# Kernel tuning notes

Measured on AMD Instinct MI355X. Metric: run time of the kernel, lower is better.

## Reference

```python
import jax, jax.numpy as jnp
import numpy as np

B, N, D, H = 16, 256, 128, 8
HD = D // H
PAIR_DIMS = [64, 64, 64]
EPS = 1e-8


def _pairwise_lv_fts(x):
    # x: [B, 4, N] four-vectors (px, py, pz, E); returns [B, N, N, 4] = (lnkt, lnz, lndelta, lnm2)
    px, py, pz, e = x[:, 0], x[:, 1], x[:, 2], x[:, 3]
    pt = jnp.sqrt(jnp.clip(px ** 2 + py ** 2, EPS))          # [B, N]
    rap = 0.5 * jnp.log1p(2.0 * pz / jnp.clip(e - pz, 1e-20))
    phi = jnp.arctan2(py, px)
    d_rap = rap[:, :, None] - rap[:, None, :]                 # [B, N, N]
    d_phi = (phi[:, :, None] - phi[:, None, :] + np.pi) % (2.0 * np.pi) - np.pi
    delta = jnp.sqrt(d_rap ** 2 + d_phi ** 2)
    lndelta = jnp.log(jnp.clip(delta, EPS))
    ptmin = jnp.minimum(pt[:, :, None], pt[:, None, :])
    lnkt = jnp.log(jnp.clip(ptmin * delta, EPS))
    lnz = jnp.log(jnp.clip(ptmin / jnp.clip(pt[:, :, None] + pt[:, None, :], EPS), EPS))
    es = e[:, :, None] + e[:, None, :]
    pxs = px[:, :, None] + px[:, None, :]
    pys = py[:, :, None] + py[:, None, :]
    pzs = pz[:, :, None] + pz[:, None, :]
    lnm2 = jnp.log(jnp.clip(es ** 2 - pxs ** 2 - pys ** 2 - pzs ** 2, EPS))
    return jnp.stack([lnkt, lnz, lndelta, lnm2], axis=-1)


def setup_inputs() -> dict:
    key = jax.random.key(0)
    ks = jax.random.split(key, 12)
    p3 = jax.random.normal(ks[0], (B, 3, N), jnp.float32)
    e = jnp.sqrt((p3 ** 2).sum(1, keepdims=True)
                 + jnp.abs(jax.random.normal(ks[1], (B, 1, N), jnp.float32)) ** 2 + 0.1)
    x_pf = jnp.concatenate([p3, e], axis=1)                   # physical four-vectors [B,4,N]
    x_feat = jax.random.normal(ks[2], (B, N, D), jnp.float32) * 0.02
    dims = [4] + PAIR_DIMS + [H]
    pw = {}
    for i in range(4):
        pw[f"pair_w{i}"] = jax.random.normal(ks[3 + i], (dims[i], dims[i + 1]), jnp.float32) / np.sqrt(dims[i])
        pw[f"pair_b{i}"] = jnp.zeros((dims[i + 1],), jnp.float32)
    proj = {n: jax.random.normal(k, (D, D), jnp.float32) / np.sqrt(D)
            for n, k in zip(["wq", "wk", "wv", "wo"], jax.random.split(ks[7], 4))}
    bias = {n: jnp.zeros((D,), jnp.float32) for n in ["bq", "bk", "bv", "bo"]}
    return dict(x_pf=x_pf, x_feat=x_feat, **pw, **proj, **bias)


def reference(x_pf, x_feat, pair_w0, pair_b0, pair_w1, pair_b1, pair_w2, pair_b2,
              pair_w3, pair_b3, wq, wk, wv, wo, bq, bk, bv, bo):
    # pairwise Lorentz-invariant features -> dense attention bias
    u = _pairwise_lv_fts(x_pf)                                # [B, N, N, 4]
    for w, b in ((pair_w0, pair_b0), (pair_w1, pair_b1), (pair_w2, pair_b2)):
        u = jax.nn.gelu(u @ w + b)
    attn_bias = jnp.transpose(u @ pair_w3 + pair_b3, (0, 3, 1, 2))  # [B, H, N, N]
    # multi-head attention with pairwise bias
    q = (x_feat @ wq + bq).reshape(B, N, H, HD)
    k = (x_feat @ wk + bk).reshape(B, N, H, HD)
    v = (x_feat @ wv + bv).reshape(B, N, H, HD)
    scores = jnp.einsum("bihd,bjhd->bhij", q, k) / np.sqrt(HD) + attn_bias
    attn = jax.nn.softmax(scores, axis=-1)
    out = jnp.einsum("bhij,bjhd->bihd", attn, v).reshape(B, N, D)
    return out @ wo + bo                                      # [B, N, D]
```

## Files before the change

kernel.cpp:

```cpp
#include <hip/hip_runtime.h>
#include <hip/hip_bf16.h>
#include <math.h>

#define B_ 16
#define N_ 256
#define D_ 128
#define H_ 8
#define HD_ 16
#define EPS_ 1e-8f
#define PI_F 3.14159265358979323846f
#define TWO_PI_F 6.28318530717958647692f
#define INV_TWO_PI_F 0.15915494309189533577f
#define L2E_F 1.4426950408889634f

#define OFF_PT   0
#define OFF_RAP  4096
#define OFF_PHI  8192
#define OFF_PX   12288
#define OFF_PY   16384
#define OFF_PZ   20480
#define OFF_E    24576
#define OFF_Q    28672
#define OFF_BIAS (28672 + 3*524288)
#define OFF_AO   (OFF_BIAS + 8388608)
#define OFF_WPACK (OFF_AO + 524288)

#define UA0  0
#define UA1H 2048
#define UA1L 6144
#define UA2H 10240
#define UA2L 14336
#define UA3H 18432
#define UA3L 19456
#define UQKV 20480

typedef _Float16 f16x8 __attribute__((ext_vector_type(8)));
typedef _Float16 f16x4 __attribute__((ext_vector_type(4)));
typedef _Float16 f16x2 __attribute__((ext_vector_type(2)));
typedef __attribute__((ext_vector_type(4))) float f4;
typedef __attribute__((ext_vector_type(4))) unsigned int u4;

__device__ __forceinline__ unsigned pkh2(float a, float b) {
    f16x2 v = { (_Float16)a, (_Float16)b };
    return __builtin_bit_cast(unsigned, v);
}
__device__ __forceinline__ float f16res(float x) {
    return x - (float)(_Float16)x;
}

__device__ __forceinline__ float gelu_f(float x) {
    float y2 = x * fmaf(0.10294337f, x * x, 2.3022079f);
    float e = __builtin_amdgcn_exp2f(-y2);
    return x * __builtin_amdgcn_rcpf(1.0f + e);
}


__global__ __launch_bounds__(256) void k_prep(
    const float* __restrict__ w0, const float* __restrict__ w1,
    const float* __restrict__ w2, const float* __restrict__ w3,
    const float* __restrict__ wq, const float* __restrict__ wk,
    const float* __restrict__ wv, const float* __restrict__ wo,
    const float* __restrict__ x_pf,
    _Float16* __restrict__ wp, float* __restrict__ ws) {
    if (blockIdx.x >= 64) {
        int idx = (blockIdx.x - 64) * 256 + threadIdx.x;
        int b = idx >> 8, n = idx & 255;
        const float* base = x_pf + (size_t)b * 4 * N_;
        float px = base[0 * N_ + n];
        float py = base[1 * N_ + n];
        float pz = base[2 * N_ + n];
        float e  = base[3 * N_ + n];
        float pt  = sqrtf(fmaxf(px * px + py * py, EPS_));
        float rap = 0.5f * log1pf(2.0f * pz / fmaxf(e - pz, 1e-20f));
        float phi = atan2f(py, px);
        ws[OFF_PT  + idx] = pt;
        ws[OFF_RAP + idx] = rap;
        ws[OFF_PHI + idx] = phi;
        ws[OFF_PX  + idx] = px;
        ws[OFF_PY  + idx] = py;
        ws[OFF_PZ  + idx] = pz;
        ws[OFF_E   + idx] = e;
        return;
    }
    int id0 = blockIdx.x * 256 + threadIdx.x;
    const int gs = 64 * 256;
    for (int e = id0; e < 2048; e += gs) {
        int fi = e >> 3, j = e & 7;
        int mt = fi >> 6, lane = fi & 63;
        int q = lane >> 4, ln = lane & 15;
        int m = mt * 16 + ln;
        _Float16 v = (_Float16)0.0f;
        if (q == 0) v = (j < 4) ? (_Float16)w0[j * 64 + m]
                                : (_Float16)f16res(w0[(j - 4) * 64 + m]);
        else if (q == 1) v = (j < 4) ? (_Float16)w0[j * 64 + m] : (_Float16)0.0f;
        wp[UA0 + e] = v;
    }
    for (int e = id0; e < 4096; e += gs) {
        int fi = e >> 3, j = e & 7;
        int mt = fi >> 7, ks = (fi >> 6) & 1, lane = fi & 63;
        int q = lane >> 4;
        int m = mt * 16 + (lane & 15);
        int k = (2 * (j >> 2) + ks) * 16 + q * 4 + (j & 3);
        float x1 = w1[k * 64 + m];
        wp[UA1H + e] = (_Float16)x1;
        wp[UA1L + e] = (_Float16)f16res(x1);
        float x2 = w2[k * 64 + m];
        wp[UA2H + e] = (_Float16)x2;
        wp[UA2L + e] = (_Float16)f16res(x2);
    }
    for (int e = id0; e < 1024; e += gs) {
        int fi = e >> 3, j = e & 7;
        int ks = fi >> 6, lane = fi & 63;
        int q = lane >> 4;
        int m = lane & 15;
        int k = (2 * (j >> 2) + ks) * 16 + q * 4 + (j & 3);
        float x = (m < 8) ? w3[k * 8 + m] : 0.0f;
        wp[UA3H + e] = (_Float16)x;
        wp[UA3L + e] = (_Float16)f16res(x);
    }
    const float* mats[4] = { wq, wk, wv, wo };
#pragma unroll 1
    for (int mi = 0; mi < 4; ++mi) {
        const float* W = mats[mi];
        _Float16* dst = wp + UQKV + mi * 32768;
        for (int e = id0; e < 16384; e += gs) {
            int fi = e >> 3, j = e & 7;
            int mt = fi >> 8, ks = (fi >> 6) & 3, lane = fi & 63;
            int k = ks * 32 + ((lane >> 4) << 3) + j;
            int o = mt * 16 + (lane & 15);
            float x = W[k * 128 + o];
            dst[e] = (_Float16)x;
            dst[16384 + e] = (_Float16)f16res(x);
        }
    }
}

__device__ __forceinline__ void epi_frag(const f4 (&acc)[4][4], const float* __restrict__ bg,
                                         int q, u4 (&Bu)[4][2]) {
#pragma unroll
    for (int mt = 0; mt < 4; ++mt) {
        f4 bv = *(const f4*)&bg[mt * 16 + q * 4];
        int ks = mt & 1, hi = (mt >> 1) * 2;
#pragma unroll
        for (int nt = 0; nt < 4; ++nt) {
            float g0 = gelu_f(acc[mt][nt][0] + bv[0]);
            float g1 = gelu_f(acc[mt][nt][1] + bv[1]);
            float g2 = gelu_f(acc[mt][nt][2] + bv[2]);
            float g3 = gelu_f(acc[mt][nt][3] + bv[3]);
            Bu[nt][ks][hi]     = pkh2(g0, g1);
            Bu[nt][ks][hi + 1] = pkh2(g2, g3);
        }
    }
}

__device__ __forceinline__ void mid_layer(f4 (&acc)[4][4],
                                          const _Float16* __restrict__ wh,
                                          const _Float16* __restrict__ wl,
                                          int lane, const u4 (&Bu)[4][2]) {
    const f4 zero4 = { 0.f, 0.f, 0.f, 0.f };
#pragma unroll
    for (int mt = 0; mt < 4; ++mt) {
        f16x8 ah0 = *(const f16x8*)&wh[((mt * 2 + 0) * 64 + lane) * 8];
        f16x8 ah1 = *(const f16x8*)&wh[((mt * 2 + 1) * 64 + lane) * 8];
        f16x8 al0 = *(const f16x8*)&wl[((mt * 2 + 0) * 64 + lane) * 8];
        f16x8 al1 = *(const f16x8*)&wl[((mt * 2 + 1) * 64 + lane) * 8];
#pragma unroll
        for (int nt = 0; nt < 4; ++nt) {
            f16x8 b0 = __builtin_bit_cast(f16x8, Bu[nt][0]);
            f16x8 b1 = __builtin_bit_cast(f16x8, Bu[nt][1]);
            f4 c = zero4;
            c = __builtin_amdgcn_mfma_f32_16x16x32_f16(ah0, b0, c, 0, 0, 0);
            c = __builtin_amdgcn_mfma_f32_16x16x32_f16(al0, b0, c, 0, 0, 0);
            c = __builtin_amdgcn_mfma_f32_16x16x32_f16(ah1, b1, c, 0, 0, 0);
            c = __builtin_amdgcn_mfma_f32_16x16x32_f16(al1, b1, c, 0, 0, 0);
            acc[mt][nt] = c;
        }
    }
}

__device__ __forceinline__ void mfma_core64x16(
    const float* __restrict__ xrow, const _Float16* __restrict__ wpm,
    int mtbase, const float* __restrict__ biasv, int lane, f4 (&cc)[4]) {
    int q = lane >> 4;
    const f4 zero4 = { 0.f, 0.f, 0.f, 0.f };
    f16x8 Bh[4], Bl[4];
#pragma unroll
    for (int ks = 0; ks < 4; ++ks) {
        const float* p = xrow + ks * 32 + q * 8;
        float4 xa = ((const float4*)p)[0];
        float4 xb = ((const float4*)p)[1];
        u4 hu = { pkh2(xa.x, xa.y), pkh2(xa.z, xa.w), pkh2(xb.x, xb.y), pkh2(xb.z, xb.w) };
        u4 lu = { pkh2(f16res(xa.x), f16res(xa.y)), pkh2(f16res(xa.z), f16res(xa.w)),
                  pkh2(f16res(xb.x), f16res(xb.y)), pkh2(f16res(xb.z), f16res(xb.w)) };
        Bh[ks] = __builtin_bit_cast(f16x8, hu);
        Bl[ks] = __builtin_bit_cast(f16x8, lu);
    }
#pragma unroll
    for (int mtl = 0; mtl < 4; ++mtl) {
        int mt = mtbase + mtl;
        f4 c = zero4;
#pragma unroll
        for (int ks = 0; ks < 4; ++ks) {
            const _Float16* fa = wpm + ((size_t)((mt * 4 + ks) * 64 + lane)) * 8;
            f16x8 ah = *(const f16x8*)fa;
            f16x8 al = *(const f16x8*)(fa + 16384);
            c = __builtin_amdgcn_mfma_f32_16x16x32_f16(ah, Bh[ks], c, 0, 0, 0);
            c = __builtin_amdgcn_mfma_f32_16x16x32_f16(ah, Bl[ks], c, 0, 0, 0);
            c = __builtin_amdgcn_mfma_f32_16x16x32_f16(al, Bh[ks], c, 0, 0, 0);
        }
        f4 bv = *(const f4*)&biasv[mtl * 16 + q * 4];
        cc[mtl] = c + bv;
    }
}

__global__ __launch_bounds__(256, 4) void k_pair_qkv(
    const float* __restrict__ ws, const _Float16* __restrict__ wp,
    const float* __restrict__ b0g, const float* __restrict__ b1g,
    const float* __restrict__ b2g, const float* __restrict__ b3g,
    float* __restrict__ bias_out,
    const float* __restrict__ xf,
    const float* __restrict__ bqv, const float* __restrict__ bkv, const float* __restrict__ bvv,
    _Float16* __restrict__ qh, _Float16* __restrict__ kh,
    _Float16* __restrict__ kl, _Float16* __restrict__ vh) {
    int tid = threadIdx.x;
    int lane = tid & 63;
    int ln = lane & 15, q = lane >> 4;

    if (blockIdx.x < 384) {
        int wid = blockIdx.x * 4 + (tid >> 6);
        int og = wid % 6, tg = wid / 6;
        int mi = og >> 1, ch = og & 1;
        const _Float16* wpm = wp + UQKV + mi * 32768;
        const float* bias = (mi == 0) ? bqv : ((mi == 1) ? bkv : bvv);
        size_t tok = (size_t)(tg * 16 + ln);
        f4 cc[4];
        mfma_core64x16(xf + tok * 128, wpm, ch * 4, bias + ch * 64, lane, cc);
        _Float16* hout = (mi == 0) ? qh : ((mi == 1) ? kh : vh);
        int b = (int)(tok >> 8), tl = (int)(tok & 255);
#pragma unroll
        for (int mtl = 0; mtl < 4; ++mtl) {
            int head = ch * 4 + mtl;
            size_t off = ((size_t)((b * 8 + head) * 256 + tl)) * 16 + q * 4;
            f16x4 hv;
#pragma unroll
            for (int r = 0; r < 4; ++r) hv[r] = (_Float16)cc[mtl][r];
            *(f16x4*)&hout[off] = hv;
            if (mi == 1) {
                f16x4 lv;
#pragma unroll
                for (int r = 0; r < 4; ++r) lv[r] = (_Float16)(cc[mtl][r] - (float)hv[r]);
                *(f16x4*)&kl[off] = lv;
            }
        }
        return;
    }

    int w2 = (blockIdx.x - 384) * 4 + (tid >> 6);
    int b = w2 / 640;
    int w = w2 - b * 640;
    int it, rr, nj;
    if (w < 256)      { it = 0; rr = w;       nj = 4; }
    else if (w < 448) { it = 1; rr = w - 256; nj = 3; }
    else if (w < 576) { it = 2; rr = w - 448; nj = 2; }
    else              { it = 3; rr = w - 576; nj = 1; }
    int i  = it * 64 + rr / nj;
    int jt = it + rr % nj;
    int j0 = jt * 64;
    int row = (b << 8) + i;

    unsigned FH01, FH23, FL01, FL23;
    {
        int ib = row;
        int jb = (b << 8) + j0 + lane;
        float pt_i = ws[OFF_PT + ib],  rap_i = ws[OFF_RAP + ib], phi_i = ws[OFF_PHI + ib];
        float px_i = ws[OFF_PX + ib],  py_i  = ws[OFF_PY  + ib];
        float pz_i = ws[OFF_PZ + ib],  e_i   = ws[OFF_E   + ib];
        float pt_j = ws[OFF_PT + jb],  rap_j = ws[OFF_RAP + jb], phi_j = ws[OFF_PHI + jb];
        float px_j = ws[OFF_PX + jb],  py_j  = ws[OFF_PY  + jb];
        float pz_j = ws[OFF_PZ + jb],  e_j   = ws[OFF_E   + jb];

        float drap = rap_i - rap_j;
        float xw = phi_i - phi_j + PI_F;
        float mw = xw - TWO_PI_F * floorf(xw * INV_TWO_PI_F);
        float dphi = mw - PI_F;
        float delta = sqrtf(drap * drap + dphi * dphi);
        float f2 = __logf(fmaxf(delta, EPS_));
        float ptmin = fminf(pt_i, pt_j);
        float f0 = __logf(fmaxf(ptmin * delta, EPS_));
        float f1 = __logf(fmaxf(ptmin / fmaxf(pt_i + pt_j, EPS_), EPS_));
        float es = e_i + e_j, pxs = px_i + px_j, pys = py_i + py_j, pzs = pz_i + pz_j;
        float f3 = __logf(fmaxf(es * es - pxs * pxs - pys * pys - pzs * pzs, EPS_));

        FH01 = pkh2(f0, f1);
        FH23 = pkh2(f2, f3);
        FL01 = pkh2(f16res(f0), f16res(f1));
        FL23 = pkh2(f16res(f2), f16res(f3));
    }

    f4 acc[4][4];
    const f4 zero4 = { 0.f, 0.f, 0.f, 0.f };

    {
        f16x8 a0[4];
#pragma unroll
        for (int mt = 0; mt < 4; ++mt)
            a0[mt] = *(const f16x8*)&wp[UA0 + (mt * 64 + lane) * 8];
#pragma unroll
        for (int nt = 0; nt < 4; ++nt) {
            int src = nt * 16 + ln;
            unsigned h01 = (unsigned)__shfl((int)FH01, src);
            unsigned h23 = (unsigned)__shfl((int)FH23, src);
            unsigned l01 = (unsigned)__shfl((int)FL01, src);
            unsigned l23 = (unsigned)__shfl((int)FL23, src);
            u4 bu;
            bu[0] = (q == 0) ? h01 : ((q == 1) ? l01 : 0u);
            bu[1] = (q == 0) ? h23 : ((q == 1) ? l23 : 0u);
            bu[2] = (q == 0) ? h01 : 0u;
            bu[3] = (q == 0) ? h23 : 0u;
            f16x8 bf = __builtin_bit_cast(f16x8, bu);
#pragma unroll
            for (int mt = 0; mt < 4; ++mt)
                acc[mt][nt] = __builtin_amdgcn_mfma_f32_16x16x32_f16(a0[mt], bf, zero4, 0, 0, 0);
        }
    }

    u4 Bu[4][2];
    epi_frag(acc, b0g, q, Bu);
    mid_layer(acc, wp + UA1H, wp + UA1L, lane, Bu);
    epi_frag(acc, b1g, q, Bu);
    mid_layer(acc, wp + UA2H, wp + UA2L, lane, Bu);
    epi_frag(acc, b2g, q, Bu);

    {
        f16x8 a3h0 = *(const f16x8*)&wp[UA3H + (0 * 64 + lane) * 8];
        f16x8 a3h1 = *(const f16x8*)&wp[UA3H + (1 * 64 + lane) * 8];
        f16x8 a3l0 = *(const f16x8*)&wp[UA3L + (0 * 64 + lane) * 8];
        f16x8 a3l1 = *(const f16x8*)&wp[UA3L + (1 * 64 + lane) * 8];
        f4 acc3[4];
#pragma unroll
        for (int nt = 0; nt < 4; ++nt) {
            f16x8 b0 = __builtin_bit_cast(f16x8, Bu[nt][0]);
            f16x8 b1 = __builtin_bit_cast(f16x8, Bu[nt][1]);
            f4 c = zero4;
            c = __builtin_amdgcn_mfma_f32_16x16x32_f16(a3h0, b0, c, 0, 0, 0);
            c = __builtin_amdgcn_mfma_f32_16x16x32_f16(a3l0, b0, c, 0, 0, 0);
            c = __builtin_amdgcn_mfma_f32_16x16x32_f16(a3h1, b1, c, 0, 0, 0);
            c = __builtin_amdgcn_mfma_f32_16x16x32_f16(a3l1, b1, c, 0, 0, 0);
            acc3[nt] = c;
        }
        if (q < 2) {
            f4 b3v = *(const f4*)&b3g[q * 4];
#pragma unroll
            for (int nt = 0; nt < 4; ++nt) {
                int jc = j0 + nt * 16 + ln;
#pragma unroll
                for (int r = 0; r < 4; ++r) {
                    int out = q * 4 + r;
                    bias_out[(((size_t)(b * H_ + out)) * N_ + i) * N_ + jc] = acc3[nt][r] + b3v[r];
                }
            }
        }
    }
}

#define SVT 264
__global__ __launch_bounds__(256) void k_attn(
    const float* __restrict__ ws,
    const _Float16* __restrict__ qh, const _Float16* __restrict__ kh,
    const _Float16* __restrict__ kl, const _Float16* __restrict__ vh,
    float* __restrict__ wso) {
    __shared__ __align__(16) _Float16 Vt[16 * SVT];
    int tid = threadIdx.x;
    int blk = blockIdx.x;
    int ib = blk & 3;
    int bh = blk >> 2;
    int b = bh >> 3;

    {
        const _Float16* vr = vh + ((size_t)(bh * 256) + tid) * 16;
        f16x8 v0 = *(const f16x8*)vr;
        f16x8 v1 = *(const f16x8*)(vr + 8);
#pragma unroll
        for (int d = 0; d < 8; ++d) {
            Vt[d * SVT + tid] = v0[d];
            Vt[(8 + d) * SVT + tid] = v1[d];
        }
    }
    __syncthreads();

    int lane = tid & 63, w = tid >> 6;
    int ln = lane & 15, q = lane >> 4;
    int i0 = ib * 64 + w * 16;
    const f4 zero4 = { 0.f, 0.f, 0.f, 0.f };

    f16x8 Bq = *(const f16x8*)&qh[((size_t)(bh * 256) + i0 + ln) * 16 + (q & 1) * 8];

    f4 accs[16];
    const _Float16* kbase = (q < 2 ? kh : kl) + ((size_t)(bh * 256)) * 16 + (q & 1) * 8;
    const float* bb = ws + OFF_BIAS + ((size_t)(bh * 256 + i0 + ln)) * 256 + q * 4;
    const float* tbb = ws + OFF_BIAS + ((size_t)bh) * 65536 + (i0 + ln);
#pragma unroll
    for (int mt = 0; mt < 16; ++mt) {
        f16x8 Ak = *(const f16x8*)&kbase[(size_t)(mt * 16 + ln) * 16];
        f4 s = __builtin_amdgcn_mfma_f32_16x16x32_f16(Ak, Bq, zero4, 0, 0, 0);
        f4 bias4;
        if ((mt >> 2) < ib) {
            const float* tb = tbb + (size_t)(mt * 16 + q * 4) * 256;
            bias4[0] = tb[0];
            bias4[1] = tb[256];
            bias4[2] = tb[512];
            bias4[3] = tb[768];
        } else {
            bias4 = *(const f4*)&bb[mt * 16];
        }
#pragma unroll
        for (int r = 0; r < 4; ++r) s[r] = fmaf(s[r], 0.25f, bias4[r]);
        accs[mt] = s;
    }

    float mx = accs[0][0];
#pragma unroll
    for (int mt = 0; mt < 16; ++mt)
#pragma unroll
        for (int r = 0; r < 4; ++r) mx = fmaxf(mx, accs[mt][r]);
    mx = fmaxf(mx, __shfl_xor(mx, 16));
    mx = fmaxf(mx, __shfl_xor(mx, 32));
    float nms = -mx * L2E_F;
    float l = 0.0f;
#pragma unroll
    for (int mt = 0; mt < 16; ++mt) {
#pragma unroll
        for (int r = 0; r < 4; ++r) {
            float p = __builtin_amdgcn_exp2f(fmaf(accs[mt][r], L2E_F, nms));
            accs[mt][r] = p;
            l += p;
        }
    }
    l += __shfl_xor(l, 16);
    l += __shfl_xor(l, 32);
    float inv = __builtin_amdgcn_rcpf(l);

    f4 o = zero4;
#pragma unroll
    for (int ks = 0; ks < 8; ++ks) {
        u4 bp = { pkh2(accs[2 * ks][0], accs[2 * ks][1]),
                  pkh2(accs[2 * ks][2], accs[2 * ks][3]),
                  pkh2(accs[2 * ks + 1][0], accs[2 * ks + 1][1]),
                  pkh2(accs[2 * ks + 1][2], accs[2 * ks + 1][3]) };
        int vb = ln * SVT + 32 * ks + 4 * q;
        f16x4 lo4 = *(const f16x4*)&Vt[vb];
        f16x4 hi4 = *(const f16x4*)&Vt[vb + 16];
        f16x8 av;
        av[0] = lo4[0]; av[1] = lo4[1]; av[2] = lo4[2]; av[3] = lo4[3];
        av[4] = hi4[0]; av[5] = hi4[1]; av[6] = hi4[2]; av[7] = hi4[3];
        o = __builtin_amdgcn_mfma_f32_16x16x32_f16(av, __builtin_bit_cast(f16x8, bp), o, 0, 0, 0);
    }
    f4 res = o * inv;
    int h = bh & 7;
    *(f4*)(wso + OFF_AO + ((size_t)(b * 256 + i0 + ln)) * 128 + h * 16 + q * 4) = res;
}

__global__ __launch_bounds__(256) void k_out(
    const float* __restrict__ ws, const _Float16* __restrict__ wp,
    const float* __restrict__ bo, float* __restrict__ out) {
    int tid = threadIdx.x;
    int lane = tid & 63, ln = lane & 15, q = lane >> 4;
    int wid = blockIdx.x * 4 + (tid >> 6);
    int og = wid & 1, tg = wid >> 1;
    const _Float16* wpm = wp + UQKV + 3 * 32768;
    size_t tok = (size_t)(tg * 16 + ln);
    f4 cc[4];
    mfma_core64x16(ws + OFF_AO + tok * 128, wpm, og * 4, bo + og * 64, lane, cc);
#pragma unroll
    for (int mtl = 0; mtl < 4; ++mtl)
        *(f4*)(out + tok * 128 + og * 64 + mtl * 16 + q * 4) = cc[mtl];
}

extern "C" void kernel_launch(void* const* d_in, const int* in_sizes, int n_in,
                              void* d_out, int out_size, void* d_ws, size_t ws_size,
                              hipStream_t stream) {
    const float* x_pf   = (const float*)d_in[0];
    const float* x_feat = (const float*)d_in[1];
    const float* w0 = (const float*)d_in[2];
    const float* b0 = (const float*)d_in[3];
    const float* w1 = (const float*)d_in[4];
    const float* b1 = (const float*)d_in[5];
    const float* w2 = (const float*)d_in[6];
    const float* b2 = (const float*)d_in[7];
    const float* w3 = (const float*)d_in[8];
    const float* b3 = (const float*)d_in[9];
    const float* wq = (const float*)d_in[10];
    const float* wk = (const float*)d_in[11];
    const float* wv = (const float*)d_in[12];
    const float* wo = (const float*)d_in[13];
    const float* bq = (const float*)d_in[14];
    const float* bk = (const float*)d_in[15];
    const float* bv = (const float*)d_in[16];
    const float* bo = (const float*)d_in[17];
    float* ws  = (float*)d_ws;
    float* out = (float*)d_out;
    _Float16* wpack = (_Float16*)(ws + OFF_WPACK);
    _Float16* qh = (_Float16*)(ws + OFF_Q);
    _Float16* kh = qh + 524288;
    _Float16* kl = kh + 524288;
    _Float16* vh = kl + 524288;

    hipLaunchKernelGGL(k_prep, dim3(80), dim3(256), 0, stream,
                       w0, w1, w2, w3, wq, wk, wv, wo, x_pf, wpack, ws);
    hipLaunchKernelGGL(k_pair_qkv, dim3(384 + 2560), dim3(256), 0, stream,
                       ws, wpack, b0, b1, b2, b3, ws + OFF_BIAS,
                       x_feat, bq, bk, bv, qh, kh, kl, vh);
    hipLaunchKernelGGL(k_attn, dim3(512), dim3(256), 0, stream, ws, qh, kh, kl, vh, ws);
    hipLaunchKernelGGL(k_out, dim3(128), dim3(256), 0, stream, ws, wpack, bo, out);
}
```

Baseline: 157.7 us.

## Split attention keys across waves with flash-style cross-wave softmax merge

The attention kernel now gives each block one 16-query tile, and its four waves each take a quarter of the 256 keys. Each wave computes a partial max, sum and output. These are merged through shared memory using rescaled exponentials, and wave 0 writes the normalized result. The grid grows from 512 to 2048 blocks to expose more parallelism and cut per-wave register use. In exchange, each block now reloads the full V tile into LDS for only 16 queries (four times as much V staging overall) and adds a barrier and a serial merge step.

```diff
diff --git a/kernel.cpp b/kernel.cpp
--- a/kernel.cpp
+++ b/kernel.cpp
@@ -370,10 +370,13 @@
     const _Float16* __restrict__ kl, const _Float16* __restrict__ vh,
     float* __restrict__ wso) {
     __shared__ __align__(16) _Float16 Vt[16 * SVT];
+    __shared__ float cm[4 * 16];
+    __shared__ float cl[4 * 16];
+    __shared__ float cO[4][16][20];
     int tid = threadIdx.x;
     int blk = blockIdx.x;
-    int ib = blk & 3;
-    int bh = blk >> 2;
+    int it = blk & 15;
+    int bh = blk >> 4;
     int b = bh >> 3;
 
     {
@@ -390,22 +393,24 @@
 
     int lane = tid & 63, w = tid >> 6;
     int ln = lane & 15, q = lane >> 4;
-    int i0 = ib * 64 + w * 16;
+    int i0 = it * 16;
     const f4 zero4 = { 0.f, 0.f, 0.f, 0.f };
 
     f16x8 Bq = *(const f16x8*)&qh[((size_t)(bh * 256) + i0 + ln) * 16 + (q & 1) * 8];
 
-    f4 accs[16];
+    f4 accs[4];
     const _Float16* kbase = (q < 2 ? kh : kl) + ((size_t)(bh * 256)) * 16 + (q & 1) * 8;
-    const float* bb = ws + OFF_BIAS + ((size_t)(bh * 256 + i0 + ln)) * 256 + q * 4;
-    const float* tbb = ws + OFF_BIAS + ((size_t)bh) * 65536 + (i0 + ln);
-#pragma unroll
-    for (int mt = 0; mt < 16; ++mt) {
-        f16x8 Ak = *(const f16x8*)&kbase[(size_t)(mt * 16 + ln) * 16];
+    bool lower = (w < (it >> 2));
+    const float* bb = ws + OFF_BIAS + ((size_t)(bh * 256 + i0 + ln)) * 256 + w * 64 + q * 4;
+    const float* tbb = ws + OFF_BIAS + ((size_t)bh) * 65536 + (size_t)(w * 64 + q * 4) * 256 + (i0 + ln);
+#pragma unroll
+    for (int mt = 0; mt < 4; ++mt) {
+        int jl = w * 64 + mt * 16 + ln;
+        f16x8 Ak = *(const f16x8*)&kbase[(size_t)jl * 16];
         f4 s = __builtin_amdgcn_mfma_f32_16x16x32_f16(Ak, Bq, zero4, 0, 0, 0);
         f4 bias4;
-        if ((mt >> 2) < ib) {
-            const float* tb = tbb + (size_t)(mt * 16 + q * 4) * 256;
+        if (lower) {
+            const float* tb = tbb + (size_t)(mt * 16) * 256;
             bias4[0] = tb[0];
             bias4[1] = tb[256];
             bias4[2] = tb[512];
@@ -420,7 +425,7 @@
 
     float mx = accs[0][0];
 #pragma unroll
-    for (int mt = 0; mt < 16; ++mt)
+    for (int mt = 0; mt < 4; ++mt)
 #pragma unroll
         for (int r = 0; r < 4; ++r) mx = fmaxf(mx, accs[mt][r]);
     mx = fmaxf(mx, __shfl_xor(mx, 16));
@@ -428,7 +433,7 @@
     float nms = -mx * L2E_F;
     float l = 0.0f;
 #pragma unroll
-    for (int mt = 0; mt < 16; ++mt) {
+    for (int mt = 0; mt < 4; ++mt) {
 #pragma unroll
         for (int r = 0; r < 4; ++r) {
             float p = __builtin_amdgcn_exp2f(fmaf(accs[mt][r], L2E_F, nms));
@@ -438,16 +443,15 @@
     }
     l += __shfl_xor(l, 16);
     l += __shfl_xor(l, 32);
-    float inv = __builtin_amdgcn_rcpf(l);
 
     f4 o = zero4;
 #pragma unroll
-    for (int ks = 0; ks < 8; ++ks) {
+    for (int ks = 0; ks < 2; ++ks) {
         u4 bp = { pkh2(accs[2 * ks][0], accs[2 * ks][1]),
                   pkh2(accs[2 * ks][2], accs[2 * ks][3]),
                   pkh2(accs[2 * ks + 1][0], accs[2 * ks + 1][1]),
                   pkh2(accs[2 * ks + 1][2], accs[2 * ks + 1][3]) };
-        int vb = ln * SVT + 32 * ks + 4 * q;
+        int vb = ln * SVT + w * 64 + 32 * ks + 4 * q;
         f16x4 lo4 = *(const f16x4*)&Vt[vb];
         f16x4 hi4 = *(const f16x4*)&Vt[vb + 16];
         f16x8 av;
@@ -455,9 +459,32 @@
         av[4] = hi4[0]; av[5] = hi4[1]; av[6] = hi4[2]; av[7] = hi4[3];
         o = __builtin_amdgcn_mfma_f32_16x16x32_f16(av, __builtin_bit_cast(f16x8, bp), o, 0, 0, 0);
     }
-    f4 res = o * inv;
-    int h = bh & 7;
-    *(f4*)(wso + OFF_AO + ((size_t)(b * 256 + i0 + ln)) * 128 + h * 16 + q * 4) = res;
+
+    if (q == 0) { cm[w * 16 + ln] = mx; cl[w * 16 + ln] = l; }
+#pragma unroll
+    for (int r = 0; r < 4; ++r) cO[w][q * 4 + r][ln] = o[r];
+    __syncthreads();
+
+    if (w == 0) {
+        float m0 = cm[ln], m1 = cm[16 + ln], m2 = cm[32 + ln], m3 = cm[48 + ln];
+        float M = fmaxf(fmaxf(m0, m1), fmaxf(m2, m3));
+        float s0 = __builtin_amdgcn_exp2f((m0 - M) * L2E_F);
+        float s1 = __builtin_amdgcn_exp2f((m1 - M) * L2E_F);
+        float s2 = __builtin_amdgcn_exp2f((m2 - M) * L2E_F);
+        float s3 = __builtin_amdgcn_exp2f((m3 - M) * L2E_F);
+        float L = s0 * cl[ln] + s1 * cl[16 + ln] + s2 * cl[32 + ln] + s3 * cl[48 + ln];
+        float inv = __builtin_amdgcn_rcpf(L);
+        f4 res;
+#pragma unroll
+        for (int r = 0; r < 4; ++r) {
+            int d = q * 4 + r;
+            float v = s0 * cO[0][d][ln] + s1 * cO[1][d][ln]
+                    + s2 * cO[2][d][ln] + s3 * cO[3][d][ln];
+            res[r] = v * inv;
+        }
+        int h = bh & 7;
+        *(f4*)(wso + OFF_AO + ((size_t)(b * 256 + i0 + ln)) * 128 + h * 16 + q * 4) = res;
+    }
 }
 
 __global__ __launch_bounds__(256) void k_out(
@@ -510,6 +537,6 @@
     hipLaunchKernelGGL(k_pair_qkv, dim3(384 + 2560), dim3(256), 0, stream,
                        ws, wpack, b0, b1, b2, b3, ws + OFF_BIAS,
                        x_feat, bq, bk, bv, qh, kh, kl, vh);
-    hipLaunchKernelGGL(k_attn, dim3(512), dim3(256), 0, stream, ws, qh, kh, kl, vh, ws);
+    hipLaunchKernelGGL(k_attn, dim3(2048), dim3(256), 0, stream, ws, qh, kh, kl, vh, ws);
     hipLaunchKernelGGL(k_out, dim3(128), dim3(256), 0, stream, ws, wpack, bo, out);
 }
```

Measured after the change: 158.2 us. Within noise of the previous version (+0.3%).
